# Kernel optimization log

Hardware: AMD Instinct MI355X
Metric: run time of the kernel (lower is better)

The kernel has to match this reference:

```python
import jax, jax.numpy as jnp
import numpy as np
from jax import lax

B, OBS, E, H = 65536, 20, 64, 64


def setup_inputs() -> dict:
    key = jax.random.key(0)
    ks = jax.random.split(key, 13)
    s = 0.1
    inp = {
        "obs_traj": jax.random.normal(ks[0], (B, OBS, 2), jnp.float32),
        "W_emb": jax.random.normal(ks[1], (E, 2), jnp.float32) * s,
        "b_emb": jax.random.normal(ks[2], (E,), jnp.float32) * s,
        "Wih_e": jax.random.normal(ks[3], (4 * H, E), jnp.float32) * s,
        "Whh_e": jax.random.normal(ks[4], (4 * H, H), jnp.float32) * s,
        "bih_e": jax.random.normal(ks[5], (4 * H,), jnp.float32) * s,
        "bhh_e": jax.random.normal(ks[6], (4 * H,), jnp.float32) * s,
        "Wih_d": jax.random.normal(ks[7], (4 * H, E), jnp.float32) * s,
        "Whh_d": jax.random.normal(ks[8], (4 * H, H), jnp.float32) * s,
        "bih_d": jax.random.normal(ks[9], (4 * H,), jnp.float32) * s,
        "bhh_d": jax.random.normal(ks[10], (4 * H,), jnp.float32) * s,
        "W_fc": jax.random.normal(ks[11], (2, H), jnp.float32) * s,
        "b_fc": jax.random.normal(ks[12], (2,), jnp.float32) * s,
        "pred_len": 12,
    }
    return inp


def _lstm_step(x, h, c, Wih, Whh, b):
    # PyTorch LSTM gate order: i, f, g, o
    g = x @ Wih.T + h @ Whh.T + b  # [B, 4H]
    i, f, gg, o = jnp.split(g, 4, axis=-1)
    c2 = jax.nn.sigmoid(f) * c + jax.nn.sigmoid(i) * jnp.tanh(gg)
    h2 = jax.nn.sigmoid(o) * jnp.tanh(c2)
    return h2, c2


def reference(obs_traj, W_emb, b_emb, Wih_e, Whh_e, bih_e, bhh_e,
              Wih_d, Whh_d, bih_d, bhh_d, W_fc, b_fc, pred_len):
    bsz = obs_traj.shape[0]
    dt = obs_traj.dtype
    # Encoder: embed all observed steps at once, then scan the LSTM over time.
    emb = jax.nn.relu(obs_traj @ W_emb.T + b_emb)  # [B, OBS, E]
    b_e = bih_e + bhh_e
    h0 = jnp.zeros((bsz, H), dt)
    c0 = jnp.zeros((bsz, H), dt)

    def enc_step(carry, x_t):
        h, c = carry
        h, c = _lstm_step(x_t, h, c, Wih_e, Whh_e, b_e)
        return (h, c), None

    (h, c), _ = lax.scan(enc_step, (h0, c0), jnp.swapaxes(emb, 0, 1))

    b_d = bih_d + bhh_d
    dec_in = jax.nn.relu(obs_traj[:, -1, :] @ W_emb.T + b_emb)  # [B, E]

    def dec_step(carry, _):
        h, c, x = carry
        h, c = _lstm_step(x, h, c, Wih_d, Whh_d, b_d)
        pred = h @ W_fc.T + b_fc  # [B, 2]
        nxt = jax.nn.relu(pred @ W_emb.T + b_emb)
        return (h, c, nxt), pred

    _, preds = lax.scan(dec_step, (h, c, dec_in), None, length=pred_len)
    return jnp.swapaxes(preds, 0, 1)  # [B, pred_len, 2]
```

## Files before the change

kernel.cpp:

```cpp
#include <hip/hip_runtime.h>

typedef __bf16 bf16x8 __attribute__((ext_vector_type(8)));
typedef __bf16 bf16x4 __attribute__((ext_vector_type(4)));
typedef float  f32x4  __attribute__((ext_vector_type(4)));
typedef float  f32x2  __attribute__((ext_vector_type(2)));

constexpr int OBS   = 20;
constexpr int PRED  = 12;
constexpr int AST   = 136;
constexpr int NBIG  = 512;
constexpr int GRID  = 768;

constexpr float SIO = -1.4426950408889634f;
constexpr float SG  =  2.8853900817779268f;

__device__ __forceinline__ float exp2_(float x) { return __builtin_amdgcn_exp2f(x); }
__device__ __forceinline__ float rcp_(float x)  { return __builtin_amdgcn_rcpf(x); }

struct SmallW {
    float  biasf_e[256];
    float  biasf_d[256];
    float4 embc[64];
    float  wfc[128];
    float  bfc[2];
};

__device__ __forceinline__ void load_bfr(bf16x8 (&bfr)[4][3],
                                         const float* Wih, const float* Whh,
                                         int wblk, int m, int q) {
    #pragma unroll
    for (int c = 0; c < 4; ++c) {
        const float sc = (c == 2) ? SG : SIO;
        const int n = c * 64 + wblk + m;
        #pragma unroll
        for (int kt = 0; kt < 3; ++kt) {
            const float* s = (kt < 2) ? (Wih + n * 64 + kt * 32 + q * 8)
                                      : (Whh + n * 64 + q * 8);
            float4 a = *(const float4*)s;
            float4 b = *(const float4*)(s + 4);
            bf16x8 v;
            v[0] = (__bf16)(sc * a.x); v[1] = (__bf16)(sc * a.y);
            v[2] = (__bf16)(sc * a.z); v[3] = (__bf16)(sc * a.w);
            v[4] = (__bf16)(sc * b.x); v[5] = (__bf16)(sc * b.y);
            v[6] = (__bf16)(sc * b.z); v[7] = (__bf16)(sc * b.w);
            bfr[c][kt] = v;
        }
    }
}

__device__ __forceinline__ void fill_wkt3(bf16x8* wkt3, const float* Whh,
                                          int wv, int lane, int wblk, int m, int q) {
    #pragma unroll
    for (int c = 0; c < 4; ++c) {
        const float sc = (c == 2) ? SG : SIO;
        const int n = c * 64 + wblk + m;
        const float* s = Whh + n * 64 + 32 + q * 8;
        float4 a = *(const float4*)s;
        float4 b = *(const float4*)(s + 4);
        bf16x8 v;
        v[0] = (__bf16)(sc * a.x); v[1] = (__bf16)(sc * a.y);
        v[2] = (__bf16)(sc * a.z); v[3] = (__bf16)(sc * a.w);
        v[4] = (__bf16)(sc * b.x); v[5] = (__bf16)(sc * b.y);
        v[6] = (__bf16)(sc * b.z); v[7] = (__bf16)(sc * b.w);
        wkt3[(wv * 4 + c) * 64 + lane] = v;
    }
}

template<int NSUB>
__device__ void lstm_body(__bf16* As, bf16x8* wkt3, float* pred_s, SmallW& sw,
                          const float* obs,
                          const float* Wih_e, const float* Whh_e,
                          const float* Wih_d, const float* Whh_d,
                          float* out, size_t gRow0)
{
    constexpr int CH = NSUB * 16;
    constexpr int NP = (NSUB + 1) / 2;
    const int tid  = threadIdx.x;
    const int wv   = tid >> 6;
    const int lane = tid & 63;
    const int m    = lane & 15;
    const int q    = lane >> 4;
    const int wblk = wv * 16;

    bf16x8 bfr[4][3];
    load_bfr(bfr, Wih_e, Whh_e, wblk, m, q);

    f32x4 cst[2 * NSUB];
    #pragma unroll
    for (int i = 0; i < 2 * NSUB; ++i) cst[i] = f32x4{0.f, 0.f, 0.f, 0.f};

    f32x4 acc[NSUB][4];

    auto gemm = [&](int chunk, const float* bfrag) {
        #pragma unroll
        for (int c = 0; c < 4; ++c) {
            f32x4 b = *(const f32x4*)&bfrag[(wv * 4 + c) * 16 + q * 4];
            #pragma unroll
            for (int s = 0; s < NSUB; ++s) acc[s][c] = b;
        }
        #pragma unroll
        for (int kt = 0; kt < 3; ++kt) {
            bf16x8 af[NSUB];
            #pragma unroll
            for (int s = 0; s < NSUB; ++s)
                af[s] = *(const bf16x8*)&As[(chunk * CH + s * 16 + m) * AST + kt * 32 + q * 8];
            #pragma unroll
            for (int s = 0; s < NSUB; ++s)
                #pragma unroll
                for (int c = 0; c < 4; ++c)
                    acc[s][c] = __builtin_amdgcn_mfma_f32_16x16x32_bf16(bfr[c][kt], af[s], acc[s][c], 0, 0, 0);
        }
        {
            bf16x8 af[NSUB];
            #pragma unroll
            for (int s = 0; s < NSUB; ++s)
                af[s] = *(const bf16x8*)&As[(chunk * CH + s * 16 + m) * AST + 96 + q * 8];
            #pragma unroll
            for (int c = 0; c < 4; ++c) {
                bf16x8 w3 = wkt3[(wv * 4 + c) * 64 + lane];
                #pragma unroll
                for (int s = 0; s < NSUB; ++s)
                    acc[s][c] = __builtin_amdgcn_mfma_f32_16x16x32_bf16(w3, af[s], acc[s][c], 0, 0, 0);
            }
        }
    };

    auto update = [&](int chunk) {
        #pragma unroll
        for (int sub = 0; sub < NSUB; ++sub) {
            const int idx = chunk * NSUB + sub;
            const int row = chunk * CH + sub * 16 + m;
            f32x4 ci = cst[idx];
            bf16x4 h4;
            #pragma unroll
            for (int r = 0; r < 4; ++r) {
                const float gi = acc[sub][0][r];
                const float gf = acc[sub][1][r];
                const float gg = acc[sub][2][r];
                const float go = acc[sub][3][r];
                const float Ef = exp2_(gf);
                const float a  = ci[r] * rcp_(1.0f + Ef);
                const float Ei = exp2_(gi);
                const float Eg = exp2_(gg);
                const float d1 = 1.0f + Ei;
                const float r1 = rcp_(fmaf(d1, Eg, d1));
                const float cN = fmaf(Eg - 1.0f, r1, a);
                const float Eo = exp2_(go);
                const float Ec = exp2_(cN * SG);
                const float d2 = 1.0f + Eo;
                const float r2 = rcp_(fmaf(d2, Ec, d2));
                const float h  = (Ec - 1.0f) * r2;
                ci[r] = cN;
                h4[r] = (__bf16)h;
            }
            cst[idx] = ci;
            *(bf16x4*)&As[row * AST + 64 + wblk + q * 4] = h4;
        }
    };

    auto emb_enc = [&](int chunk, int t) {
        const int h8 = lane >> 5;
        #pragma unroll
        for (int p = 0; p < NP; ++p) {
            const int rloc = p * 32 + (lane & 31);
            if (rloc < CH) {
                const int row = chunk * CH + rloc;
                f32x2 ov = *(const f32x2*)(obs + (gRow0 + row) * (OBS * 2) + t * 2);
                bf16x8 v;
                #pragma unroll
                for (int j = 0; j < 8; ++j) {
                    float4 wc = sw.embc[wblk + h8 * 8 + j];
                    v[j] = (__bf16)fmaxf(fmaf(ov[0], wc.x, fmaf(ov[1], wc.y, wc.z)), 0.f);
                }
                *(bf16x8*)&As[row * AST + wblk + h8 * 8] = v;
            }
        }
    };

    __syncthreads();

    emb_enc(0, 0);
    emb_enc(1, 0);
    __syncthreads();
    gemm(0, sw.biasf_e);

    for (int t = 0; t < OBS; ++t) {
        __syncthreads();
        update(0);
        gemm(1, sw.biasf_e);
        if (t + 1 < OBS) emb_enc(0, t + 1);
        __syncthreads();
        update(1);
        if (t + 1 < OBS) {
            gemm(0, sw.biasf_e);
            emb_enc(1, t + 1);
        }
    }

    load_bfr(bfr, Wih_d, Whh_d, wblk, m, q);
    fill_wkt3(wkt3, Whh_d, wv, lane, wblk, m, q);
    gemm(0, sw.biasf_d);

    auto pred_phase = [&](int chunk, int td) {
        const int comp = (tid >> 2) & 1;
        const int seg  = tid & 3;
        #pragma unroll
        for (int p = 0; p < NP; ++p) {
            const int rloc = p * 32 + (tid >> 3);
            const int row  = chunk * CH + rloc;
            const bool act = (rloc < CH);
            float pv = 0.f;
            if (act) {
                bf16x8 h0 = *(const bf16x8*)&As[row * AST + 64 + seg * 16];
                bf16x8 h1 = *(const bf16x8*)&As[row * AST + 64 + seg * 16 + 8];
                f32x4 w0 = *(const f32x4*)&sw.wfc[comp * 64 + seg * 16];
                f32x4 w1 = *(const f32x4*)&sw.wfc[comp * 64 + seg * 16 + 4];
                f32x4 w2 = *(const f32x4*)&sw.wfc[comp * 64 + seg * 16 + 8];
                f32x4 w3 = *(const f32x4*)&sw.wfc[comp * 64 + seg * 16 + 12];
                pv = (float)h0[0] * w0[0] + (float)h0[1] * w0[1] + (float)h0[2] * w0[2] + (float)h0[3] * w0[3]
                   + (float)h0[4] * w1[0] + (float)h0[5] * w1[1] + (float)h0[6] * w1[2] + (float)h0[7] * w1[3]
                   + (float)h1[0] * w2[0] + (float)h1[1] * w2[1] + (float)h1[2] * w2[2] + (float)h1[3] * w2[3]
                   + (float)h1[4] * w3[0] + (float)h1[5] * w3[1] + (float)h1[6] * w3[2] + (float)h1[7] * w3[3];
            }
            pv += __shfl_xor(pv, 1, 64);
            pv += __shfl_xor(pv, 2, 64);
            if (act && seg == 0) {
                pv += sw.bfc[comp];
                pred_s[row * 2 + comp] = pv;
                out[((gRow0 + row) * PRED + td) * 2 + comp] = pv;
            }
        }
    };
    auto emb_dec = [&](int chunk) {
        const int h8 = lane >> 5;
        #pragma unroll
        for (int p = 0; p < NP; ++p) {
            const int rloc = p * 32 + (lane & 31);
            if (rloc < CH) {
                const int row = chunk * CH + rloc;
                f32x2 pv = *(const f32x2*)&pred_s[row * 2];
                bf16x8 v;
                #pragma unroll
                for (int j = 0; j < 8; ++j) {
                    float4 wc = sw.embc[wblk + h8 * 8 + j];
                    v[j] = (__bf16)fmaxf(fmaf(pv[0], wc.x, fmaf(pv[1], wc.y, wc.z)), 0.f);
                }
                *(bf16x8*)&As[row * AST + wblk + h8 * 8] = v;
            }
        }
    };

    for (int td = 0; td < PRED; ++td) {
        __syncthreads();
        update(0);
        gemm(1, sw.biasf_d);
        __syncthreads();
        update(1);
        pred_phase(0, td);
        __syncthreads();
        pred_phase(1, td);
        if (td + 1 < PRED) emb_dec(0);
        __syncthreads();
        if (td + 1 < PRED) {
            emb_dec(1);
            gemm(0, sw.biasf_d);
        }
    }
}

__global__ __launch_bounds__(256, 3)
void vanilla_lstm(const float* __restrict__ obs,
                  const float* __restrict__ W_emb, const float* __restrict__ b_emb,
                  const float* __restrict__ Wih_e, const float* __restrict__ Whh_e,
                  const float* __restrict__ bih_e, const float* __restrict__ bhh_e,
                  const float* __restrict__ Wih_d, const float* __restrict__ Whh_d,
                  const float* __restrict__ bih_d, const float* __restrict__ bhh_d,
                  const float* __restrict__ W_fc,  const float* __restrict__ b_fc,
                  float* __restrict__ out)
{
    __shared__ __align__(16) __bf16 As[96 * AST];
    __shared__ bf16x8 wkt3[1024];
    __shared__ __align__(16) float  pred_s[96 * 2];
    __shared__ SmallW sw;

    const int tid = threadIdx.x;

    {
        const int wv_ = tid >> 6, c_ = (tid >> 4) & 3, qr = tid & 15;
        const int g = c_ * 64 + wv_ * 16 + qr;
        const float sc = (c_ == 2) ? SG : SIO;
        sw.biasf_e[tid] = sc * (bih_e[g] + bhh_e[g]);
        sw.biasf_d[tid] = sc * (bih_d[g] + bhh_d[g]);
    }
    if (tid < 64)  sw.embc[tid] = make_float4(W_emb[2 * tid], W_emb[2 * tid + 1], b_emb[tid], 0.f);
    if (tid < 128) sw.wfc[tid]  = W_fc[tid];
    if (tid < 2)   sw.bfc[tid]  = b_fc[tid];

    {
        uint4 z; z.x = z.y = z.z = z.w = 0u;
        #pragma unroll
        for (int i = 0; i < 3; ++i) {
            const int idx = tid + i * 256;
            const int r = idx >> 3, o = idx & 7;
            *((uint4*)&As[r * AST + 64] + o) = z;
        }
    }

    {
        const int wv = tid >> 6, lane = tid & 63, m = lane & 15, q = lane >> 4;
        fill_wkt3(wkt3, Whh_e, wv, lane, wv * 16, m, q);
    }

    const int bid = blockIdx.x;
    if (bid < NBIG) {
        lstm_body<3>(As, wkt3, pred_s, sw, obs, Wih_e, Whh_e, Wih_d, Whh_d,
                     out, (size_t)bid * 96);
    } else {
        lstm_body<2>(As, wkt3, pred_s, sw, obs, Wih_e, Whh_e, Wih_d, Whh_d,
                     out, (size_t)NBIG * 96 + (size_t)(bid - NBIG) * 64);
    }
}

extern "C" void kernel_launch(void* const* d_in, const int* in_sizes, int n_in,
                              void* d_out, int out_size, void* d_ws, size_t ws_size,
                              hipStream_t stream) {
    (void)in_sizes; (void)n_in; (void)d_ws; (void)ws_size; (void)out_size;
    const float* obs   = (const float*)d_in[0];
    const float* W_emb = (const float*)d_in[1];
    const float* b_emb = (const float*)d_in[2];
    const float* Wih_e = (const float*)d_in[3];
    const float* Whh_e = (const float*)d_in[4];
    const float* bih_e = (const float*)d_in[5];
    const float* bhh_e = (const float*)d_in[6];
    const float* Wih_d = (const float*)d_in[7];
    const float* Whh_d = (const float*)d_in[8];
    const float* bih_d = (const float*)d_in[9];
    const float* bhh_d = (const float*)d_in[10];
    const float* W_fc  = (const float*)d_in[11];
    const float* b_fc  = (const float*)d_in[12];
    float* o = (float*)d_out;

    dim3 grid(GRID), block(256);
    hipLaunchKernelGGL(vanilla_lstm, grid, block, 0, stream,
                       obs, W_emb, b_emb, Wih_e, Whh_e, bih_e, bhh_e,
                       Wih_d, Whh_d, bih_d, bhh_d, W_fc, b_fc, o);
}
```

Measured before the change: 281.1 us.

## Fold FC head into decoder embedding via MFMA and prefetch obs loads

```diff
diff --git a/kernel.cpp b/kernel.cpp
--- a/kernel.cpp
+++ b/kernel.cpp
@@ -67,7 +67,7 @@
 }
 
 template<int NSUB>
-__device__ void lstm_body(__bf16* As, bf16x8* wkt3, float* pred_s, SmallW& sw,
+__device__ void lstm_body(__bf16* As, bf16x8* wkt3, SmallW& sw,
                           const float* obs,
                           const float* Wih_e, const float* Whh_e,
                           const float* Wih_d, const float* Whh_d,
@@ -158,19 +158,26 @@
         }
     };
 
-    auto emb_enc = [&](int chunk, int t) {
+    auto load_obs = [&](int chunk, int t, f32x2* ov) {
+        #pragma unroll
+        for (int p = 0; p < NP; ++p) {
+            const int rloc = p * 32 + (lane & 31);
+            if (rloc < CH)
+                ov[p] = *(const f32x2*)(obs + (gRow0 + chunk * CH + rloc) * (OBS * 2) + t * 2);
+        }
+    };
+    auto emb_store = [&](int chunk, const f32x2* ov) {
         const int h8 = lane >> 5;
         #pragma unroll
         for (int p = 0; p < NP; ++p) {
             const int rloc = p * 32 + (lane & 31);
             if (rloc < CH) {
                 const int row = chunk * CH + rloc;
-                f32x2 ov = *(const f32x2*)(obs + (gRow0 + row) * (OBS * 2) + t * 2);
                 bf16x8 v;
                 #pragma unroll
                 for (int j = 0; j < 8; ++j) {
                     float4 wc = sw.embc[wblk + h8 * 8 + j];
-                    v[j] = (__bf16)fmaxf(fmaf(ov[0], wc.x, fmaf(ov[1], wc.y, wc.z)), 0.f);
+                    v[j] = (__bf16)fmaxf(fmaf(ov[p][0], wc.x, fmaf(ov[p][1], wc.y, wc.z)), 0.f);
                 }
                 *(bf16x8*)&As[row * AST + wblk + h8 * 8] = v;
             }
@@ -179,27 +186,71 @@
 
     __syncthreads();
 
-    emb_enc(0, 0);
-    emb_enc(1, 0);
+    {
+        f32x2 o0[NP], o1[NP];
+        load_obs(0, 0, o0); load_obs(1, 0, o1);
+        emb_store(0, o0);   emb_store(1, o1);
+    }
     __syncthreads();
     gemm(0, sw.biasf_e);
 
     for (int t = 0; t < OBS; ++t) {
         __syncthreads();
+        f32x2 ovA[NP];
+        if (t + 1 < OBS) load_obs(0, t + 1, ovA);
         update(0);
         gemm(1, sw.biasf_e);
-        if (t + 1 < OBS) emb_enc(0, t + 1);
-        __syncthreads();
+        if (t + 1 < OBS) emb_store(0, ovA);
+        __syncthreads();
+        f32x2 ovB[NP];
+        if (t + 1 < OBS) load_obs(1, t + 1, ovB);
         update(1);
         if (t + 1 < OBS) {
             gemm(0, sw.biasf_e);
-            emb_enc(1, t + 1);
+            emb_store(1, ovB);
         }
     }
 
     load_bfr(bfr, Wih_d, Whh_d, wblk, m, q);
     fill_wkt3(wkt3, Whh_d, wv, lane, wblk, m, q);
-    gemm(0, sw.biasf_d);
+
+    bf16x8 wcf[2];
+    {
+        float4 we = sw.embc[wblk + m];
+        #pragma unroll
+        for (int kt = 0; kt < 2; ++kt) {
+            bf16x8 v;
+            #pragma unroll
+            for (int j = 0; j < 8; ++j) {
+                const int k = kt * 32 + q * 8 + j;
+                v[j] = (__bf16)(we.x * sw.wfc[k] + we.y * sw.wfc[64 + k]);
+            }
+            wcf[kt] = v;
+        }
+    }
+    f32x4 bcf;
+    #pragma unroll
+    for (int r = 0; r < 4; ++r) {
+        float4 wc = sw.embc[wblk + q * 4 + r];
+        bcf[r] = wc.x * sw.bfc[0] + wc.y * sw.bfc[1] + wc.z;
+    }
+
+    auto emb_gemm = [&](int chunk) {
+        #pragma unroll
+        for (int s = 0; s < NSUB; ++s) {
+            const int row = chunk * CH + s * 16 + m;
+            f32x4 a = bcf;
+            #pragma unroll
+            for (int kt = 0; kt < 2; ++kt) {
+                bf16x8 hf = *(const bf16x8*)&As[row * AST + 64 + kt * 32 + q * 8];
+                a = __builtin_amdgcn_mfma_f32_16x16x32_bf16(wcf[kt], hf, a, 0, 0, 0);
+            }
+            bf16x4 x4;
+            #pragma unroll
+            for (int r = 0; r < 4; ++r) x4[r] = (__bf16)fmaxf(a[r], 0.f);
+            *(bf16x4*)&As[row * AST + wblk + q * 4] = x4;
+        }
+    };
 
     auto pred_phase = [&](int chunk, int td) {
         const int comp = (tid >> 2) & 1;
@@ -226,29 +277,12 @@
             pv += __shfl_xor(pv, 2, 64);
             if (act && seg == 0) {
                 pv += sw.bfc[comp];
-                pred_s[row * 2 + comp] = pv;
                 out[((gRow0 + row) * PRED + td) * 2 + comp] = pv;
             }
         }
     };
-    auto emb_dec = [&](int chunk) {
-        const int h8 = lane >> 5;
-        #pragma unroll
-        for (int p = 0; p < NP; ++p) {
-            const int rloc = p * 32 + (lane & 31);
-            if (rloc < CH) {
-                const int row = chunk * CH + rloc;
-                f32x2 pv = *(const f32x2*)&pred_s[row * 2];
-                bf16x8 v;
-                #pragma unroll
-                for (int j = 0; j < 8; ++j) {
-                    float4 wc = sw.embc[wblk + h8 * 8 + j];
-                    v[j] = (__bf16)fmaxf(fmaf(pv[0], wc.x, fmaf(pv[1], wc.y, wc.z)), 0.f);
-                }
-                *(bf16x8*)&As[row * AST + wblk + h8 * 8] = v;
-            }
-        }
-    };
+
+    gemm(0, sw.biasf_d);
 
     for (int td = 0; td < PRED; ++td) {
         __syncthreads();
@@ -256,15 +290,14 @@
         gemm(1, sw.biasf_d);
         __syncthreads();
         update(1);
+        if (td + 1 < PRED) emb_gemm(0);
         pred_phase(0, td);
         __syncthreads();
+        if (td + 1 < PRED) {
+            emb_gemm(1);
+            gemm(0, sw.biasf_d);
+        }
         pred_phase(1, td);
-        if (td + 1 < PRED) emb_dec(0);
-        __syncthreads();
-        if (td + 1 < PRED) {
-            emb_dec(1);
-            gemm(0, sw.biasf_d);
-        }
     }
 }
 
@@ -280,7 +313,6 @@
 {
     __shared__ __align__(16) __bf16 As[96 * AST];
     __shared__ bf16x8 wkt3[1024];
-    __shared__ __align__(16) float  pred_s[96 * 2];
     __shared__ SmallW sw;
 
     const int tid = threadIdx.x;
@@ -313,10 +345,10 @@
 
     const int bid = blockIdx.x;
     if (bid < NBIG) {
-        lstm_body<3>(As, wkt3, pred_s, sw, obs, Wih_e, Whh_e, Wih_d, Whh_d,
+        lstm_body<3>(As, wkt3, sw, obs, Wih_e, Whh_e, Wih_d, Whh_d,
                      out, (size_t)bid * 96);
     } else {
-        lstm_body<2>(As, wkt3, pred_s, sw, obs, Wih_e, Whh_e, Wih_d, Whh_d,
+        lstm_body<2>(As, wkt3, sw, obs, Wih_e, Whh_e, Wih_d, Whh_d,
                      out, (size_t)NBIG * 96 + (size_t)(bid - NBIG) * 64);
     }
 }
```

New measurement: 271.8 us. 3.3% less time.
